# Kernel tuning notes

Measured on AMD Instinct MI355X. Metric: run time of the kernel, lower is better.

The kernel has to match this reference:

```python
import jax, jax.numpy as jnp
import numpy as np

# Static conv / spline hyperparameters (match init_kwargs)
KH = KW = 3
SH = SW = 1          # stride
DH = DW = 1          # dilation
GRID_SIZE = 5
SPLINE_ORDER = 3
N_CONVS = 8


def _extract_patches(x):
    """im2col unfold. x: (B,C,H,W) -> (B,C,Ho,Wo,KH*KW), valid padding."""
    B, C, H, W = x.shape
    Ho = (H - (KH - 1) * DH - 1) // SH + 1
    Wo = (W - (KW - 1) * DW - 1) // SW + 1
    cols = []
    for i in range(KH):
        for j in range(KW):
            cols.append(x[:, :,
                          i * DH: i * DH + (Ho - 1) * SH + 1: SH,
                          j * DW: j * DW + (Wo - 1) * SW + 1: SW])
    return jnp.stack(cols, axis=-1), Ho, Wo


def _b_splines(xf, grid):
    """Cox-de Boor recursion. xf: (P,K), grid: (K, G+2*so+1) -> (P,K,G+so)."""
    x = xf[:, :, None]
    bases = ((x >= grid[:, :-1]) & (x < grid[:, 1:])).astype(xf.dtype)
    for k in range(1, SPLINE_ORDER + 1):
        bases = ((x - grid[:, :-(k + 1)]) / (grid[:, k:-1] - grid[:, :-(k + 1)])
                 * bases[:, :, :-1]
                 + (grid[:, k + 1:] - x) / (grid[:, k + 1:] - grid[:, 1:-k])
                 * bases[:, :, 1:])
    return bases


def setup_inputs() -> dict:
    key = jax.random.key(0)
    k0, k1, k2, k3 = jax.random.split(key, 4)
    B, C, H, W = 8, 32, 64, 64
    K = KH * KW                       # in_features of KANLinear = 9
    coeff = GRID_SIZE + SPLINE_ORDER  # spline coefficients per input = 8
    # activations inside grid_range [-1, 1]
    x = jax.random.uniform(k0, (B, C, H, W), jnp.float32, -1.0, 1.0)
    # grid buffer: arange(-so, gs+so+1)*h + grid_range[0], tiled per input feature
    h = (1.0 - (-1.0)) / GRID_SIZE
    g = jnp.arange(-SPLINE_ORDER, GRID_SIZE + SPLINE_ORDER + 1,
                   dtype=jnp.float32) * h - 1.0
    grid = jnp.tile(g[None, :], (K, 1))  # (K, 12)
    base_weight = jax.random.normal(k1, (N_CONVS, K), jnp.float32) / np.sqrt(K)
    spline_weight = jax.random.normal(k2, (N_CONVS, K, coeff), jnp.float32) * 0.1
    spline_scaler = jax.random.normal(k3, (N_CONVS, K), jnp.float32) / np.sqrt(K) + 1.0
    return {"x": x, "grid": grid, "base_weight": base_weight,
            "spline_weight": spline_weight, "spline_scaler": spline_scaler}


def reference(x, grid, base_weight, spline_weight, spline_scaler):
    B, C, H, W = x.shape
    patches, Ho, Wo = _extract_patches(x)          # (B,C,Ho,Wo,K)
    K = KH * KW
    xf = patches.reshape(-1, K)                    # (P, K), P = B*C*Ho*Wo
    # KANLinear: base path (SiLU + linear) + spline path (B-spline basis + linear)
    base_out = jnp.einsum('pk,vk->pv', jax.nn.silu(xf), base_weight)
    bases = _b_splines(xf, grid)                   # (P, K, coeff)
    scaled_sw = spline_weight * spline_scaler[:, :, None]
    spline_out = jnp.einsum('pkc,vkc->pv', bases, scaled_sw)
    out = (base_out + spline_out).reshape(B, C, Ho, Wo, N_CONVS)
    # channel-major then conv ordering: out[:, kern + channel*n_convs]
    return out.transpose(0, 1, 4, 2, 3).reshape(B, C * N_CONVS, Ho, Wo)
```

## Files before the change

kernel.cpp:

```cpp
#include <hip/hip_runtime.h>

typedef _Float16 f16;
typedef _Float16 f16x8 __attribute__((ext_vector_type(8)));
typedef float    f32x4 __attribute__((ext_vector_type(4)));

#define HO 62
#define WO 62

__global__ __launch_bounds__(256, 5) void kan_conv_nobar(
    const float* __restrict__ x,
    const float* __restrict__ grid,
    const float* __restrict__ bw,
    const float* __restrict__ sw,
    const float* __restrict__ sc,
    float* __restrict__ out)
{
    __shared__ __align__(16) f16 feat[4 * 2880];

    const int tid  = threadIdx.x;
    const int lane = tid & 63;
    const int w    = tid >> 6;
    f16* wfeat = &feat[w * 2880];

    const int bx    = blockIdx.x;
    const int plane = bx >> 3;
    const int chunk = bx & 7;
    const int r0    = chunk * 8;
    const int c0    = w * 16;

    const int nn = lane & 15;
    const int kb = lane >> 4;
    f16x8 bfrag[3][2];
    #pragma unroll
    for (int ki = 0; ki < 3; ++ki) {
        #pragma unroll
        for (int kjp = 0; kjp < 2; ++kjp) {
            f16x8 bf;
            #pragma unroll
            for (int e = 0; e < 8; ++e) {
                const int k    = kb * 8 + e;
                const int kj   = kjp * 2 + (k >> 4);
                const int slot = k & 15;
                float wv = 0.0f;
                if (nn < 8 && kj < 3 && slot < 9) {
                    const int kk = ki * 3 + kj;
                    wv = (slot == 0) ? bw[nn * 9 + kk]
                                     : sw[(nn * 9 + kk) * 8 + (slot - 1)] * sc[nn * 9 + kk];
                }
                bf[e] = (f16)wv;
            }
            bfrag[ki][kjp] = bf;
        }
    }

    const float* xp = x + (size_t)plane * 4096;
    float xv3[3];
    int   p3[3];
    #pragma unroll
    for (int it = 0; it < 3; ++it) {
        int p = it * 64 + lane;
        p3[it] = p;
        int row = p / 18;
        int col = p - row * 18;
        int gy = r0 + row; gy = (gy < 64) ? gy : 63;
        int gx = c0 + col; gx = (gx < 64) ? gx : 63;
        xv3[it] = xp[gy * 64 + gx];
    }

    const float g0    = grid[0];
    const float inv_h = 1.0f / (grid[1] - grid[0]);

    #pragma unroll
    for (int it = 0; it < 3; ++it) {
        const int p = p3[it];
        if (p < 180) {
            const float xv = xv3[it];
            const float s = xv / (1.0f + __expf(-xv));
            const float u = (xv - g0) * inv_h;
            int j = (int)floorf(u);
            j = (j < 3) ? 3 : ((j > 7) ? 7 : j);
            const float t   = u - (float)j;
            const float omt = 1.0f - t;
            const float t2  = t * t;
            const float t3  = t2 * t;
            const float c6  = 1.0f / 6.0f;
            float bv0 = omt * omt * omt * c6;
            float bv1 = (3.0f * t3 - 6.0f * t2 + 4.0f) * c6;
            float bv2 = (-3.0f * t3 + 3.0f * t2 + 3.0f * t + 1.0f) * c6;
            float bv3 = t3 * c6;

            f16* fp = &wfeat[p * 16];
            f16x8 z0 = {(f16)s, (f16)0.f, (f16)0.f, (f16)0.f,
                        (f16)0.f, (f16)0.f, (f16)0.f, (f16)0.f};
            f16x8 z1 = {(f16)0.f, (f16)0.f, (f16)0.f, (f16)0.f,
                        (f16)0.f, (f16)0.f, (f16)0.f, (f16)0.f};
            *(f16x8*)fp       = z0;
            *(f16x8*)(fp + 8) = z1;
            fp[j - 2] = (f16)bv0;
            fp[j - 1] = (f16)bv1;
            fp[j]     = (f16)bv2;
            fp[j + 1] = (f16)bv3;
        }
    }

    const int mI    = lane & 15;
    const int khalf = kb & 1;
    const int cAdd  = kb >> 1;
    const int aBase = (mI + cAdd) * 16 + khalf * 8;

    f16x8 af[3][2];
    #pragma unroll
    for (int kjp = 0; kjp < 2; ++kjp) {
        af[0][kjp] = *(const f16x8*)&wfeat[aBase + kjp * 32 + 0 * 288];
        af[1][kjp] = *(const f16x8*)&wfeat[aBase + kjp * 32 + 1 * 288];
    }

    #pragma unroll
    for (int i = 0; i < 8; ++i) {
        #pragma unroll
        for (int kjp = 0; kjp < 2; ++kjp)
            af[(i + 2) % 3][kjp] =
                *(const f16x8*)&wfeat[aBase + kjp * 32 + (i + 2) * 288];

        f32x4 acc = {0.f, 0.f, 0.f, 0.f};
        #pragma unroll
        for (int ki = 0; ki < 3; ++ki) {
            #pragma unroll
            for (int kjp = 0; kjp < 2; ++kjp)
                acc = __builtin_amdgcn_mfma_f32_16x16x32_f16(
                          af[(i + ki) % 3][kjp], bfrag[ki][kjp], acc, 0, 0, 0);
        }

        const int ho = r0 + i;
        if (nn < 8 && ho < HO) {
            const int cb = c0 + kb * 4;
            float* po = out + ((size_t)(plane * 8 + nn) * (HO * WO)) + ho * WO + cb;
            if (cb + 3 < WO) {
                float2 lo = {acc[0], acc[1]};
                float2 hi = {acc[2], acc[3]};
                *(float2*)po       = lo;
                *(float2*)(po + 2) = hi;
            } else {
                #pragma unroll
                for (int q = 0; q < 4; ++q)
                    if (cb + q < WO) po[q] = acc[q];
            }
        }
    }
}

extern "C" void kernel_launch(void* const* d_in, const int* in_sizes, int n_in,
                              void* d_out, int out_size, void* d_ws, size_t ws_size,
                              hipStream_t stream) {
    const float* x    = (const float*)d_in[0];
    const float* grid = (const float*)d_in[1];
    const float* bw   = (const float*)d_in[2];
    const float* sw   = (const float*)d_in[3];
    const float* sc   = (const float*)d_in[4];
    float* out = (float*)d_out;

    kan_conv_nobar<<<2048, 256, 0, stream>>>(x, grid, bw, sw, sc, out);
}
```

Baseline: 94.27 us.

## Precompute packed f16 weight fragments in a prep kernel and load per wave

Adds a tiny prep kernel that builds the f16 MFMA B-fragments (base weight plus scaled spline weights) once into workspace. The main kernel then loads six f16x8 vectors per lane instead of each wave doing scattered fp32 loads and multiplies. The work-unit index is also remapped so each wave owns one plane/chunk/column slice, and a zero pad is added after each LDS slice. Occupancy launch bound drops from 5 to 4 blocks, and the extra launch adds a serial dependency.

```diff
diff --git a/kernel.cpp b/kernel.cpp
--- a/kernel.cpp
+++ b/kernel.cpp
@@ -7,76 +7,80 @@
 #define HO 62
 #define WO 62
 
-__global__ __launch_bounds__(256, 5) void kan_conv_nobar(
+__global__ __launch_bounds__(384) void kan_prep(
+    const float* __restrict__ bw, const float* __restrict__ sw,
+    const float* __restrict__ sc, f16x8* __restrict__ ws)
+{
+    const int tid  = threadIdx.x;
+    const int lane = tid & 63;
+    const int q    = tid >> 6;
+    const int ki   = q >> 1;
+    const int kjp  = q & 1;
+    const int nn   = lane & 15;
+    const int kb   = lane >> 4;
+    f16x8 bf;
+    #pragma unroll
+    for (int e = 0; e < 8; ++e) {
+        const int k    = kb * 8 + e;
+        const int kj   = kjp * 2 + (k >> 4);
+        const int slot = k & 15;
+        float wv = 0.0f;
+        if (nn < 8 && kj < 3 && slot < 9) {
+            const int kk = ki * 3 + kj;
+            wv = (slot == 0) ? bw[nn * 9 + kk]
+                             : sw[(nn * 9 + kk) * 8 + (slot - 1)] * sc[nn * 9 + kk];
+        }
+        bf[e] = (f16)wv;
+    }
+    ws[q * 64 + lane] = bf;
+}
+
+#define SLICE 2896
+__global__ __launch_bounds__(256, 4) void kan_main(
     const float* __restrict__ x,
-    const float* __restrict__ grid,
-    const float* __restrict__ bw,
-    const float* __restrict__ sw,
-    const float* __restrict__ sc,
+    const float* __restrict__ grid_,
+    const f16x8* __restrict__ ws,
     float* __restrict__ out)
 {
-    __shared__ __align__(16) f16 feat[4 * 2880];
+    __shared__ __align__(16) f16 feat[4 * SLICE];
 
     const int tid  = threadIdx.x;
     const int lane = tid & 63;
     const int w    = tid >> 6;
-    f16* wfeat = &feat[w * 2880];
+    f16* wfeat = &feat[w * SLICE];
 
-    const int bx    = blockIdx.x;
-    const int plane = bx >> 3;
-    const int chunk = bx & 7;
+    const int unit  = blockIdx.x * 4 + w;
+    const int plane = unit >> 5;
+    const int chunk = (unit >> 2) & 7;
+    const int s     = unit & 3;
     const int r0    = chunk * 8;
-    const int c0    = w * 16;
+    const int c0    = s * 16;
 
-    const int nn = lane & 15;
-    const int kb = lane >> 4;
     f16x8 bfrag[3][2];
     #pragma unroll
-    for (int ki = 0; ki < 3; ++ki) {
-        #pragma unroll
-        for (int kjp = 0; kjp < 2; ++kjp) {
-            f16x8 bf;
-            #pragma unroll
-            for (int e = 0; e < 8; ++e) {
-                const int k    = kb * 8 + e;
-                const int kj   = kjp * 2 + (k >> 4);
-                const int slot = k & 15;
-                float wv = 0.0f;
-                if (nn < 8 && kj < 3 && slot < 9) {
-                    const int kk = ki * 3 + kj;
-                    wv = (slot == 0) ? bw[nn * 9 + kk]
-                                     : sw[(nn * 9 + kk) * 8 + (slot - 1)] * sc[nn * 9 + kk];
-                }
-                bf[e] = (f16)wv;
-            }
-            bfrag[ki][kjp] = bf;
-        }
-    }
+    for (int q = 0; q < 6; ++q)
+        bfrag[q >> 1][q & 1] = ws[q * 64 + lane];
 
-    const float* xp = x + (size_t)plane * 4096;
-    float xv3[3];
-    int   p3[3];
-    #pragma unroll
-    for (int it = 0; it < 3; ++it) {
-        int p = it * 64 + lane;
-        p3[it] = p;
-        int row = p / 18;
-        int col = p - row * 18;
-        int gy = r0 + row; gy = (gy < 64) ? gy : 63;
-        int gx = c0 + col; gx = (gx < 64) ? gx : 63;
-        xv3[it] = xp[gy * 64 + gx];
-    }
+    if (lane < 2)
+        *(f16x8*)&wfeat[2880 + lane * 8] = (f16x8){(f16)0.f,(f16)0.f,(f16)0.f,(f16)0.f,
+                                                   (f16)0.f,(f16)0.f,(f16)0.f,(f16)0.f};
 
-    const float g0    = grid[0];
-    const float inv_h = 1.0f / (grid[1] - grid[0]);
+    const float g0    = grid_[0];
+    const float inv_h = 1.0f / (grid_[1] - grid_[0]);
+    const float* xp   = x + (size_t)plane * 4096;
 
     #pragma unroll
     for (int it = 0; it < 3; ++it) {
-        const int p = p3[it];
+        const int p = it * 64 + lane;
         if (p < 180) {
-            const float xv = xv3[it];
-            const float s = xv / (1.0f + __expf(-xv));
-            const float u = (xv - g0) * inv_h;
+            const int row = p / 18;
+            const int col = p - row * 18;
+            int gy = r0 + row; gy = (gy < 64) ? gy : 63;
+            int gx = c0 + col; gx = (gx < 64) ? gx : 63;
+            const float xv = xp[gy * 64 + gx];
+
+            const float si = xv / (1.0f + __expf(-xv));
+            const float u  = (xv - g0) * inv_h;
             int j = (int)floorf(u);
             j = (j < 3) ? 3 : ((j > 7) ? 7 : j);
             const float t   = u - (float)j;
@@ -84,13 +88,13 @@
             const float t2  = t * t;
             const float t3  = t2 * t;
             const float c6  = 1.0f / 6.0f;
-            float bv0 = omt * omt * omt * c6;
-            float bv1 = (3.0f * t3 - 6.0f * t2 + 4.0f) * c6;
-            float bv2 = (-3.0f * t3 + 3.0f * t2 + 3.0f * t + 1.0f) * c6;
-            float bv3 = t3 * c6;
+            const float bv0 = omt * omt * omt * c6;
+            const float bv1 = (3.0f * t3 - 6.0f * t2 + 4.0f) * c6;
+            const float bv2 = (-3.0f * t3 + 3.0f * t2 + 3.0f * t + 1.0f) * c6;
+            const float bv3 = t3 * c6;
 
             f16* fp = &wfeat[p * 16];
-            f16x8 z0 = {(f16)s, (f16)0.f, (f16)0.f, (f16)0.f,
+            f16x8 z0 = {(f16)si, (f16)0.f, (f16)0.f, (f16)0.f,
                         (f16)0.f, (f16)0.f, (f16)0.f, (f16)0.f};
             f16x8 z1 = {(f16)0.f, (f16)0.f, (f16)0.f, (f16)0.f,
                         (f16)0.f, (f16)0.f, (f16)0.f, (f16)0.f};
@@ -104,6 +108,8 @@
     }
 
     const int mI    = lane & 15;
+    const int kb    = lane >> 4;
+    const int nn    = mI;
     const int khalf = kb & 1;
     const int cAdd  = kb >> 1;
     const int aBase = (mI + cAdd) * 16 + khalf * 8;
@@ -124,12 +130,11 @@
 
         f32x4 acc = {0.f, 0.f, 0.f, 0.f};
         #pragma unroll
-        for (int ki = 0; ki < 3; ++ki) {
+        for (int ki = 0; ki < 3; ++ki)
             #pragma unroll
             for (int kjp = 0; kjp < 2; ++kjp)
                 acc = __builtin_amdgcn_mfma_f32_16x16x32_f16(
                           af[(i + ki) % 3][kjp], bfrag[ki][kjp], acc, 0, 0, 0);
-        }
 
         const int ho = r0 + i;
         if (nn < 8 && ho < HO) {
@@ -158,6 +163,8 @@
     const float* sw   = (const float*)d_in[3];
     const float* sc   = (const float*)d_in[4];
     float* out = (float*)d_out;
+    f16x8* ws  = (f16x8*)d_ws;
 
-    kan_conv_nobar<<<2048, 256, 0, stream>>>(x, grid, bw, sw, sc, out);
+    kan_prep<<<1, 384, 0, stream>>>(bw, sw, sc, ws);
+    kan_main<<<2048, 256, 0, stream>>>(x, grid, ws, out);
 }
```

Result: faster. 79.52 us (-15.6%).
